# Performance work log

Hardware: AMD Instinct MI355X
Metric: run time of the kernel (lower is better)

## Reference

```python
import jax, jax.numpy as jnp
import numpy as np

N = 100000
E = 1600000
D_IN = 128
D_OUT = 128


def setup_inputs() -> dict:
    key = jax.random.key(0)
    k1, k2, k3, k4 = jax.random.split(key, 4)
    x = jax.random.normal(k1, (N, D_IN), dtype=jnp.float32)
    edge_index = jax.random.randint(k2, (2, E), 0, N, dtype=jnp.int64)
    edge_weight = jax.random.uniform(k3, (E,), dtype=jnp.float32)
    # PyG Linear (glorot) weight stored as [in, out] so that xw = x @ weight
    weight = jax.random.normal(k4, (D_IN, D_OUT), dtype=jnp.float32) * (1.0 / np.sqrt(D_IN))
    bias = jnp.zeros((D_OUT,), dtype=jnp.float32)
    prelu_a = jnp.full((1,), 0.25, dtype=jnp.float32)  # nn.PReLU default
    return {"x": x, "edge_index": edge_index, "edge_weight": edge_weight,
            "weight": weight, "bias": bias, "prelu_a": prelu_a}


def _gcn_forward(x, edge_index, edge_weight, weight, bias, prelu_a):
    n = x.shape[0]
    # Linear transform first (PyG GCNConv applies lin before propagate)
    xw = x @ weight  # [N, D_OUT]

    # gcn_norm: add self-loops with weight 1.0
    loop = jnp.arange(n, dtype=edge_index.dtype)
    row = jnp.concatenate([edge_index[0], loop])  # source
    col = jnp.concatenate([edge_index[1], loop])  # target
    ew = jnp.concatenate([edge_weight, jnp.ones((n,), dtype=edge_weight.dtype)])

    # symmetric normalization: deg computed at targets
    deg = jax.ops.segment_sum(ew, col, num_segments=n)  # [N]
    dinv = jnp.where(deg > 0, jax.lax.rsqrt(deg), 0.0)
    norm = dinv[row] * ew * dinv[col]  # [E+N]

    # gather-scale-scatter aggregation
    msgs = norm[:, None] * xw[row]  # [E+N, D_OUT]
    out = jax.ops.segment_sum(msgs, col, num_segments=n) + bias

    # PReLU (single shared slope)
    return jnp.where(out >= 0, out, prelu_a[0] * out)


def reference(x, edge_index, edge_weight, weight, bias, prelu_a):
    return _gcn_forward(x, edge_index, edge_weight, weight, bias, prelu_a)
```

## Files before the change

### kernel.cpp

```cpp
#include <hip/hip_runtime.h>
#include <hip/hip_bf16.h>

#define D 128
#define NBMAX 512
#define CURPAD 16
#define BCAP 6144

typedef __attribute__((ext_vector_type(8))) short bf16x8;
typedef __attribute__((ext_vector_type(4))) float f32x4;

__device__ inline unsigned short f2bf(float f) {
    unsigned u = __float_as_uint(f);
    u = (u + 0x7FFFu + ((u >> 16) & 1u)) >> 16;
    return (unsigned short)u;
}
__device__ inline float bf2f_lo(unsigned u) { return __uint_as_float(u << 16); }
__device__ inline float bf2f_hi(unsigned u) { return __uint_as_float(u & 0xFFFF0000u); }

__global__ __launch_bounds__(512) void prep(int* __restrict__ bcursor, int NB,
                                            const float* __restrict__ W,
                                            bf16x8* __restrict__ gW,
                                            const float* __restrict__ bias,
                                            float* __restrict__ bias_perm) {
    int tid = threadIdx.x;
    if (blockIdx.x == 0) {
        for (int i = tid; i < NB * CURPAD; i += 512) bcursor[i] = 0;
        if (tid < 128) {
            int l = tid >> 3, j = tid & 7;
            bias_perm[tid] = bias[l + 16 * j];
        }
    } else {
        for (int idx = tid; idx < 2048; idx += 512) {
            int tile = idx >> 6;
            int ln   = idx & 63;
            int kt   = tile >> 3;
            int ct   = tile & 7;
            int k0   = kt * 32 + (ln >> 4) * 8;
            int nn   = ct * 16 + (ln & 15);
            bf16x8 v;
            #pragma unroll
            for (int j = 0; j < 8; ++j) v[j] = (short)f2bf(W[(k0 + j) * D + nn]);
            gW[idx] = v;
        }
    }
}

__global__ __launch_bounds__(1024) void phase1(const int* __restrict__ rowi,
                                               const int* __restrict__ coli,
                                               const float* __restrict__ ew,
                                               int* __restrict__ bcursor,
                                               int2* __restrict__ tmp, int E) {
    __shared__ int hist[4][NBMAX];
    __shared__ int runbase[4][NBMAX];
    int tid = threadIdx.x;
    int par = tid >> 8;
    for (int i = tid; i < 4 * NBMAX; i += 1024) ((int*)hist)[i] = 0;
    __syncthreads();
    int base = blockIdx.x * 8192 + tid * 8;
    int col[8], row[8], rank[8]; float w[8];
    if (base + 8 <= E) {
        int4 c0 = *(const int4*)(coli + base), c1 = *(const int4*)(coli + base + 4);
        int4 r0 = *(const int4*)(rowi + base), r1 = *(const int4*)(rowi + base + 4);
        float4 w0 = *(const float4*)(ew + base), w1 = *(const float4*)(ew + base + 4);
        col[0]=c0.x; col[1]=c0.y; col[2]=c0.z; col[3]=c0.w;
        col[4]=c1.x; col[5]=c1.y; col[6]=c1.z; col[7]=c1.w;
        row[0]=r0.x; row[1]=r0.y; row[2]=r0.z; row[3]=r0.w;
        row[4]=r1.x; row[5]=r1.y; row[6]=r1.z; row[7]=r1.w;
        w[0]=w0.x; w[1]=w0.y; w[2]=w0.z; w[3]=w0.w;
        w[4]=w1.x; w[5]=w1.y; w[6]=w1.z; w[7]=w1.w;
    } else {
        #pragma unroll
        for (int j = 0; j < 8; ++j) {
            int e = base + j;
            if (e < E) { col[j] = coli[e]; row[j] = rowi[e]; w[j] = ew[e]; }
            else       { col[j] = -1; }
        }
    }
    #pragma unroll
    for (int j = 0; j < 8; ++j) {
        if (col[j] >= 0) rank[j] = atomicAdd(&hist[par][col[j] >> 8], 1);
    }
    __syncthreads();
    for (int i = tid; i < NBMAX; i += 1024) {
        int c0 = hist[0][i], c1 = hist[1][i], c2 = hist[2][i], c3 = hist[3][i];
        int tot = c0 + c1 + c2 + c3;
        int b = tot ? atomicAdd(&bcursor[i * CURPAD], tot) : 0;
        runbase[0][i] = b;
        runbase[1][i] = b + c0;
        runbase[2][i] = b + c0 + c1;
        runbase[3][i] = b + c0 + c1 + c2;
    }
    __syncthreads();
    #pragma unroll
    for (int j = 0; j < 8; ++j) {
        if (col[j] >= 0) {
            int b = col[j] >> 8;
            int off = runbase[par][b] + rank[j];
            if (off < BCAP)
                tmp[(size_t)b * BCAP + off] =
                    make_int2(((col[j] & 255) << 24) | row[j], __float_as_int(w[j]));
        }
    }
}

__global__ __launch_bounds__(256) void phase2(int2* __restrict__ tmp,
                                              const int* __restrict__ bcursor,
                                              int* __restrict__ rowptr, int* __restrict__ cnt,
                                              float* __restrict__ dinv, int N) {
    __shared__ int2 ebuf[BCAP];
    __shared__ unsigned int cnt_s[2][256];
    __shared__ unsigned long long deg_s[2][256];
    __shared__ int scan_s[256];
    __shared__ int cur[2][256];
    int tid = threadIdx.x;
    int par = tid >> 7;
    cnt_s[0][tid] = 0; cnt_s[1][tid] = 0;
    deg_s[0][tid] = 0; deg_s[1][tid] = 0;
    __syncthreads();
    int b = blockIdx.x;
    int count = bcursor[b * CURPAD]; if (count > BCAP) count = BCAP;
    int gbase = b * BCAP;
    for (int e = tid * 2; e < count; e += 512) {
        if (e + 1 < count) {
            int4 q = *(const int4*)(tmp + gbase + e);
            int2 v0 = make_int2(q.x, q.y), v1 = make_int2(q.z, q.w);
            ebuf[e] = v0; ebuf[e + 1] = v1;
            unsigned cof0 = ((unsigned)v0.x) >> 24, cof1 = ((unsigned)v1.x) >> 24;
            atomicAdd(&cnt_s[par][cof0], 1u);
            atomicAdd(&cnt_s[par][cof1], 1u);
            atomicAdd(&deg_s[par][cof0],
                (unsigned long long)(__int_as_float(v0.y) * 1048576.0f + 0.5f));
            atomicAdd(&deg_s[par][cof1],
                (unsigned long long)(__int_as_float(v1.y) * 1048576.0f + 0.5f));
        } else {
            int2 v = tmp[gbase + e];
            ebuf[e] = v;
            unsigned cof = ((unsigned)v.x) >> 24;
            atomicAdd(&cnt_s[par][cof], 1u);
            atomicAdd(&deg_s[par][cof],
                (unsigned long long)(__int_as_float(v.y) * 1048576.0f + 0.5f));
        }
    }
    __syncthreads();
    int c0 = (int)cnt_s[0][tid];
    int v0 = c0 + (int)cnt_s[1][tid];
    scan_s[tid] = v0; __syncthreads();
    for (int off = 1; off < 256; off <<= 1) {
        int t = (tid >= off) ? scan_s[tid - off] : 0;
        __syncthreads(); scan_s[tid] += t; __syncthreads();
    }
    int excl = scan_s[tid] - v0;
    int node = b * 256 + tid;
    if (node < N) {
        rowptr[node] = gbase + excl;
        cnt[node] = v0;
        unsigned long long dsum = deg_s[0][tid] + deg_s[1][tid];
        float deg = 1.0f + (float)((double)dsum * (1.0 / 1048576.0));
        dinv[node] = rsqrtf(deg);
    }
    cur[0][tid] = gbase + excl;
    cur[1][tid] = gbase + excl + c0;
    __syncthreads();
    int glimit = gbase + count;
    for (int e = tid * 2; e < count; e += 512) {
        int2 v = ebuf[e];
        unsigned coff = ((unsigned)v.x) >> 24;
        int pos = atomicAdd(&cur[par][coff], 1);
        if (pos < glimit) tmp[pos] = make_int2(v.x & 0xFFFFFF, v.y);
        if (e + 1 < count) {
            int2 v1 = ebuf[e + 1];
            unsigned cof1 = ((unsigned)v1.x) >> 24;
            int pos1 = atomicAdd(&cur[par][cof1], 1);
            if (pos1 < glimit) tmp[pos1] = make_int2(v1.x & 0xFFFFFF, v1.y);
        }
    }
}

__global__ __launch_bounds__(256) void gemm_mfma(const float* __restrict__ x,
                                                 const bf16x8* __restrict__ gW,
                                                 const float* __restrict__ dinv,
                                                 unsigned short* __restrict__ yw, int N) {
    int tid  = threadIdx.x;
    int wid  = tid >> 6;
    int lane = tid & 63;
    int quad = lane >> 4;
    int m16  = lane & 15;
    int row0 = blockIdx.x * 64 + wid * 16;
    int row  = row0 + m16;

    f32x4 acc[8];
    #pragma unroll
    for (int ct = 0; ct < 8; ++ct) acc[ct] = (f32x4){0.f, 0.f, 0.f, 0.f};

    #pragma unroll
    for (int kt = 0; kt < 4; ++kt) {
        bf16x8 a;
        if (row < N) {
            const float* xp = x + (size_t)row * D + kt * 32 + quad * 8;
            float4 u0 = *(const float4*)xp;
            float4 u1 = *(const float4*)(xp + 4);
            a[0] = (short)f2bf(u0.x); a[1] = (short)f2bf(u0.y);
            a[2] = (short)f2bf(u0.z); a[3] = (short)f2bf(u0.w);
            a[4] = (short)f2bf(u1.x); a[5] = (short)f2bf(u1.y);
            a[6] = (short)f2bf(u1.z); a[7] = (short)f2bf(u1.w);
        } else {
            #pragma unroll
            for (int j = 0; j < 8; ++j) a[j] = 0;
        }
        #pragma unroll
        for (int ct = 0; ct < 8; ++ct) {
            acc[ct] = __builtin_amdgcn_mfma_f32_16x16x32_bf16(
                a, gW[(kt * 8 + ct) * 64 + lane], acc[ct], 0, 0, 0);
        }
    }

    int rq = row0 + quad * 4;
    #pragma unroll
    for (int i = 0; i < 4; ++i) {
        int r = rq + i;
        if (r < N) {
            float sc = dinv[r];
            unsigned p0 = (unsigned)f2bf(sc * acc[0][i]) | ((unsigned)f2bf(sc * acc[1][i]) << 16);
            unsigned p1 = (unsigned)f2bf(sc * acc[2][i]) | ((unsigned)f2bf(sc * acc[3][i]) << 16);
            unsigned p2 = (unsigned)f2bf(sc * acc[4][i]) | ((unsigned)f2bf(sc * acc[5][i]) << 16);
            unsigned p3 = (unsigned)f2bf(sc * acc[6][i]) | ((unsigned)f2bf(sc * acc[7][i]) << 16);
            *(uint4*)(yw + (size_t)r * D + m16 * 8) = make_uint4(p0, p1, p2, p3);
        }
    }
}

__global__ __launch_bounds__(256) void aggregate(const unsigned short* __restrict__ yw,
                                                 const float* __restrict__ dinv,
                                                 const int* __restrict__ rowptr,
                                                 const int* __restrict__ cnt,
                                                 const int2* __restrict__ sorted,
                                                 const float* __restrict__ bias_perm,
                                                 const float* __restrict__ prelu_a,
                                                 float* __restrict__ out, int N) {
    int wid  = threadIdx.x >> 6;
    int lane = threadIdx.x & 63;
    int n = blockIdx.x * 4 + wid;
    if (n >= N) return;
    int g = lane >> 4;
    int l = lane & 15;
    float2 a0 = {0.f,0.f}, a1 = {0.f,0.f}, a2 = {0.f,0.f}, a3 = {0.f,0.f};
    int s = rowptr[n];
    int cn = cnt[n];
    for (int base = 0; base < cn; base += 64) {
        int rem = cn - base;
        int m = rem < 64 ? rem : 64;
        int2 er = make_int2(0, 0);
        if (lane < rem) er = sorted[s + base + lane];
        float ewv = __int_as_float(er.y);
        int idx = g;
        int   r0 = __shfl(er.x, idx);
        float w0 = __shfl(ewv, idx);
        if (idx >= m) w0 = 0.f;
        uint4 v0 = *(const uint4*)(yw + (size_t)r0 * D + l * 8);
        for (int j = 4; j < m; j += 4) {
            int idx1 = j + g;
            int   r1 = __shfl(er.x, idx1);
            float w1 = __shfl(ewv, idx1);
            if (idx1 >= m) w1 = 0.f;
            uint4 v1 = *(const uint4*)(yw + (size_t)r1 * D + l * 8);
            a0.x = fmaf(w0, bf2f_lo(v0.x), a0.x); a0.y = fmaf(w0, bf2f_hi(v0.x), a0.y);
            a1.x = fmaf(w0, bf2f_lo(v0.y), a1.x); a1.y = fmaf(w0, bf2f_hi(v0.y), a1.y);
            a2.x = fmaf(w0, bf2f_lo(v0.z), a2.x); a2.y = fmaf(w0, bf2f_hi(v0.z), a2.y);
            a3.x = fmaf(w0, bf2f_lo(v0.w), a3.x); a3.y = fmaf(w0, bf2f_hi(v0.w), a3.y);
            v0 = v1; w0 = w1;
        }
        a0.x = fmaf(w0, bf2f_lo(v0.x), a0.x); a0.y = fmaf(w0, bf2f_hi(v0.x), a0.y);
        a1.x = fmaf(w0, bf2f_lo(v0.y), a1.x); a1.y = fmaf(w0, bf2f_hi(v0.y), a1.y);
        a2.x = fmaf(w0, bf2f_lo(v0.z), a2.x); a2.y = fmaf(w0, bf2f_hi(v0.z), a2.y);
        a3.x = fmaf(w0, bf2f_lo(v0.w), a3.x); a3.y = fmaf(w0, bf2f_hi(v0.w), a3.y);
    }
    a0.x += __shfl_xor(a0.x, 16); a0.y += __shfl_xor(a0.y, 16);
    a1.x += __shfl_xor(a1.x, 16); a1.y += __shfl_xor(a1.y, 16);
    a2.x += __shfl_xor(a2.x, 16); a2.y += __shfl_xor(a2.y, 16);
    a3.x += __shfl_xor(a3.x, 16); a3.y += __shfl_xor(a3.y, 16);
    a0.x += __shfl_xor(a0.x, 32); a0.y += __shfl_xor(a0.y, 32);
    a1.x += __shfl_xor(a1.x, 32); a1.y += __shfl_xor(a1.y, 32);
    a2.x += __shfl_xor(a2.x, 32); a2.y += __shfl_xor(a2.y, 32);
    a3.x += __shfl_xor(a3.x, 32); a3.y += __shfl_xor(a3.y, 32);

    if (lane < 16) {
        uint4 sv = *(const uint4*)(yw + (size_t)n * D + lane * 8);
        a0.x += bf2f_lo(sv.x); a0.y += bf2f_hi(sv.x);
        a1.x += bf2f_lo(sv.y); a1.y += bf2f_hi(sv.y);
        a2.x += bf2f_lo(sv.z); a2.y += bf2f_hi(sv.z);
        a3.x += bf2f_lo(sv.w); a3.y += bf2f_hi(sv.w);
        float di = dinv[n];
        float pa = prelu_a[0];
        float4 b0 = *(const float4*)(bias_perm + lane * 8);
        float4 b1 = *(const float4*)(bias_perm + lane * 8 + 4);
        float av[8] = {a0.x, a0.y, a1.x, a1.y, a2.x, a2.y, a3.x, a3.y};
        float bb[8] = {b0.x, b0.y, b0.z, b0.w, b1.x, b1.y, b1.z, b1.w};
        float* op = out + (size_t)n * D + lane;
        #pragma unroll
        for (int j = 0; j < 8; ++j) {
            float v = fmaf(di, av[j], bb[j]);
            v = (v >= 0.f) ? v : pa * v;
            op[16 * j] = v;
        }
    }
}

extern "C" void kernel_launch(void* const* d_in, const int* in_sizes, int n_in,
                              void* d_out, int out_size, void* d_ws, size_t ws_size,
                              hipStream_t stream) {
    const float* x       = (const float*)d_in[0];
    const int*   ei      = (const int*)d_in[1];
    const float* ew      = (const float*)d_in[2];
    const float* W       = (const float*)d_in[3];
    const float* bias    = (const float*)d_in[4];
    const float* prelu_a = (const float*)d_in[5];
    float* out = (float*)d_out;

    int N = in_sizes[0] / D;
    int E = in_sizes[2];
    const int* rowi = ei;
    const int* coli = ei + E;
    int NB = (N + 255) >> 8;

    char* ws = (char*)d_ws;
    size_t o = 0;
    int2*  tmp = (int2*)(ws + o); o += (size_t)NB * BCAP * 8;
    unsigned short* yw = (unsigned short*)(ws + o); o += (size_t)N * D * 2;
    bf16x8* gW   = (bf16x8*)(ws + o); o += 2048 * 16;
    float* bias_perm = (float*)(ws + o); o += D * 4;
    int* bcursor = (int*)(ws + o); o += (size_t)NB * CURPAD * 4;
    o = (o + 255) & ~(size_t)255;
    int* rowptr  = (int*)(ws + o); o += (size_t)N * 4;
    int* cnt     = (int*)(ws + o); o += (size_t)N * 4;
    float* dinv  = (float*)(ws + o); o += (size_t)N * 4;

    prep<<<2, 512, 0, stream>>>(bcursor, NB, W, gW, bias, bias_perm);
    phase1<<<(E + 8191) / 8192, 1024, 0, stream>>>(rowi, coli, ew, bcursor, tmp, E);
    phase2<<<NB, 256, 0, stream>>>(tmp, bcursor, rowptr, cnt, dinv, N);
    gemm_mfma<<<(N + 63) / 64, 256, 0, stream>>>(x, gW, dinv, yw, N);
    aggregate<<<(N + 3) / 4, 256, 0, stream>>>(yw, dinv, rowptr, cnt, tmp, bias_perm, prelu_a, out, N);
}
```

Before: 228.7 us.

## Drop LDS edge buffer in phase2, sort into separate array, fold prep into phase2

```diff
diff --git a/kernel.cpp b/kernel.cpp
--- a/kernel.cpp
+++ b/kernel.cpp
@@ -4,7 +4,7 @@
 #define D 128
 #define NBMAX 512
 #define CURPAD 16
-#define BCAP 6144
+#define BCAP 4608
 
 typedef __attribute__((ext_vector_type(8))) short bf16x8;
 typedef __attribute__((ext_vector_type(4))) float f32x4;
@@ -17,20 +17,74 @@
 __device__ inline float bf2f_lo(unsigned u) { return __uint_as_float(u << 16); }
 __device__ inline float bf2f_hi(unsigned u) { return __uint_as_float(u & 0xFFFF0000u); }
 
-__global__ __launch_bounds__(512) void prep(int* __restrict__ bcursor, int NB,
-                                            const float* __restrict__ W,
-                                            bf16x8* __restrict__ gW,
-                                            const float* __restrict__ bias,
-                                            float* __restrict__ bias_perm) {
+__global__ __launch_bounds__(1024) void phase1(const int* __restrict__ rowi,
+                                               const int* __restrict__ coli,
+                                               const float* __restrict__ ew,
+                                               int* __restrict__ bcursor,
+                                               int2* __restrict__ tmp, int E) {
+    __shared__ int hist[4][NBMAX];
+    __shared__ int runbase[4][NBMAX];
     int tid = threadIdx.x;
-    if (blockIdx.x == 0) {
-        for (int i = tid; i < NB * CURPAD; i += 512) bcursor[i] = 0;
-        if (tid < 128) {
-            int l = tid >> 3, j = tid & 7;
-            bias_perm[tid] = bias[l + 16 * j];
-        }
+    int par = tid >> 8;
+    for (int i = tid; i < 4 * NBMAX; i += 1024) ((int*)hist)[i] = 0;
+    __syncthreads();
+    int base = blockIdx.x * 4096 + tid * 4;
+    int col[4], row[4], rank[4]; float w[4];
+    if (base + 4 <= E) {
+        int4 c = *(const int4*)(coli + base);
+        int4 r = *(const int4*)(rowi + base);
+        float4 f = *(const float4*)(ew + base);
+        col[0]=c.x; col[1]=c.y; col[2]=c.z; col[3]=c.w;
+        row[0]=r.x; row[1]=r.y; row[2]=r.z; row[3]=r.w;
+        w[0]=f.x; w[1]=f.y; w[2]=f.z; w[3]=f.w;
     } else {
-        for (int idx = tid; idx < 2048; idx += 512) {
+        #pragma unroll
+        for (int j = 0; j < 4; ++j) {
+            int e = base + j;
+            if (e < E) { col[j] = coli[e]; row[j] = rowi[e]; w[j] = ew[e]; }
+            else       { col[j] = -1; }
+        }
+    }
+    #pragma unroll
+    for (int j = 0; j < 4; ++j) {
+        if (col[j] >= 0) rank[j] = atomicAdd(&hist[par][col[j] >> 8], 1);
+    }
+    __syncthreads();
+    for (int i = tid; i < NBMAX; i += 1024) {
+        int c0 = hist[0][i], c1 = hist[1][i], c2 = hist[2][i], c3 = hist[3][i];
+        int tot = c0 + c1 + c2 + c3;
+        int b = tot ? atomicAdd(&bcursor[i * CURPAD], tot) : 0;
+        runbase[0][i] = b;
+        runbase[1][i] = b + c0;
+        runbase[2][i] = b + c0 + c1;
+        runbase[3][i] = b + c0 + c1 + c2;
+    }
+    __syncthreads();
+    #pragma unroll
+    for (int j = 0; j < 4; ++j) {
+        if (col[j] >= 0) {
+            int b = col[j] >> 8;
+            int off = runbase[par][b] + rank[j];
+            if (off < BCAP)
+                tmp[(size_t)b * BCAP + off] =
+                    make_int2(((col[j] & 255) << 24) | row[j], __float_as_int(w[j]));
+        }
+    }
+}
+
+__global__ __launch_bounds__(256) void phase2(const int2* __restrict__ tmp,
+                                              int2* __restrict__ sorted,
+                                              const int* __restrict__ bcursor,
+                                              int* __restrict__ rowptr, int* __restrict__ cnt,
+                                              float* __restrict__ dinv, int N, int NB,
+                                              const float* __restrict__ W,
+                                              bf16x8* __restrict__ gW,
+                                              const float* __restrict__ bias,
+                                              float* __restrict__ bias_perm) {
+    int tid = threadIdx.x;
+    int b = blockIdx.x;
+    if (b == NB) {
+        for (int idx = tid; idx < 2048; idx += 256) {
             int tile = idx >> 6;
             int ln   = idx & 63;
             int kt   = tile >> 3;
@@ -42,103 +96,38 @@
             for (int j = 0; j < 8; ++j) v[j] = (short)f2bf(W[(k0 + j) * D + nn]);
             gW[idx] = v;
         }
-    }
-}
-
-__global__ __launch_bounds__(1024) void phase1(const int* __restrict__ rowi,
-                                               const int* __restrict__ coli,
-                                               const float* __restrict__ ew,
-                                               int* __restrict__ bcursor,
-                                               int2* __restrict__ tmp, int E) {
-    __shared__ int hist[4][NBMAX];
-    __shared__ int runbase[4][NBMAX];
-    int tid = threadIdx.x;
-    int par = tid >> 8;
-    for (int i = tid; i < 4 * NBMAX; i += 1024) ((int*)hist)[i] = 0;
-    __syncthreads();
-    int base = blockIdx.x * 8192 + tid * 8;
-    int col[8], row[8], rank[8]; float w[8];
-    if (base + 8 <= E) {
-        int4 c0 = *(const int4*)(coli + base), c1 = *(const int4*)(coli + base + 4);
-        int4 r0 = *(const int4*)(rowi + base), r1 = *(const int4*)(rowi + base + 4);
-        float4 w0 = *(const float4*)(ew + base), w1 = *(const float4*)(ew + base + 4);
-        col[0]=c0.x; col[1]=c0.y; col[2]=c0.z; col[3]=c0.w;
-        col[4]=c1.x; col[5]=c1.y; col[6]=c1.z; col[7]=c1.w;
-        row[0]=r0.x; row[1]=r0.y; row[2]=r0.z; row[3]=r0.w;
-        row[4]=r1.x; row[5]=r1.y; row[6]=r1.z; row[7]=r1.w;
-        w[0]=w0.x; w[1]=w0.y; w[2]=w0.z; w[3]=w0.w;
-        w[4]=w1.x; w[5]=w1.y; w[6]=w1.z; w[7]=w1.w;
-    } else {
-        #pragma unroll
-        for (int j = 0; j < 8; ++j) {
-            int e = base + j;
-            if (e < E) { col[j] = coli[e]; row[j] = rowi[e]; w[j] = ew[e]; }
-            else       { col[j] = -1; }
-        }
-    }
-    #pragma unroll
-    for (int j = 0; j < 8; ++j) {
-        if (col[j] >= 0) rank[j] = atomicAdd(&hist[par][col[j] >> 8], 1);
-    }
-    __syncthreads();
-    for (int i = tid; i < NBMAX; i += 1024) {
-        int c0 = hist[0][i], c1 = hist[1][i], c2 = hist[2][i], c3 = hist[3][i];
-        int tot = c0 + c1 + c2 + c3;
-        int b = tot ? atomicAdd(&bcursor[i * CURPAD], tot) : 0;
-        runbase[0][i] = b;
-        runbase[1][i] = b + c0;
-        runbase[2][i] = b + c0 + c1;
-        runbase[3][i] = b + c0 + c1 + c2;
-    }
-    __syncthreads();
-    #pragma unroll
-    for (int j = 0; j < 8; ++j) {
-        if (col[j] >= 0) {
-            int b = col[j] >> 8;
-            int off = runbase[par][b] + rank[j];
-            if (off < BCAP)
-                tmp[(size_t)b * BCAP + off] =
-                    make_int2(((col[j] & 255) << 24) | row[j], __float_as_int(w[j]));
-        }
-    }
-}
-
-__global__ __launch_bounds__(256) void phase2(int2* __restrict__ tmp,
-                                              const int* __restrict__ bcursor,
-                                              int* __restrict__ rowptr, int* __restrict__ cnt,
-                                              float* __restrict__ dinv, int N) {
-    __shared__ int2 ebuf[BCAP];
+        if (tid < 128) {
+            int l = tid >> 3, j = tid & 7;
+            bias_perm[tid] = bias[l + 16 * j];
+        }
+        return;
+    }
     __shared__ unsigned int cnt_s[2][256];
     __shared__ unsigned long long deg_s[2][256];
     __shared__ int scan_s[256];
     __shared__ int cur[2][256];
-    int tid = threadIdx.x;
     int par = tid >> 7;
     cnt_s[0][tid] = 0; cnt_s[1][tid] = 0;
     deg_s[0][tid] = 0; deg_s[1][tid] = 0;
     __syncthreads();
-    int b = blockIdx.x;
     int count = bcursor[b * CURPAD]; if (count > BCAP) count = BCAP;
     int gbase = b * BCAP;
-    for (int e = tid * 2; e < count; e += 512) {
-        if (e + 1 < count) {
-            int4 q = *(const int4*)(tmp + gbase + e);
-            int2 v0 = make_int2(q.x, q.y), v1 = make_int2(q.z, q.w);
-            ebuf[e] = v0; ebuf[e + 1] = v1;
-            unsigned cof0 = ((unsigned)v0.x) >> 24, cof1 = ((unsigned)v1.x) >> 24;
-            atomicAdd(&cnt_s[par][cof0], 1u);
-            atomicAdd(&cnt_s[par][cof1], 1u);
-            atomicAdd(&deg_s[par][cof0],
-                (unsigned long long)(__int_as_float(v0.y) * 1048576.0f + 0.5f));
-            atomicAdd(&deg_s[par][cof1],
-                (unsigned long long)(__int_as_float(v1.y) * 1048576.0f + 0.5f));
+    for (int e0 = tid * 4; e0 < count; e0 += 1024) {
+        int m = count - e0; if (m > 4) m = 4;
+        int2 v[4];
+        if (m == 4) {
+            int4 q0 = *(const int4*)(tmp + gbase + e0);
+            int4 q1 = *(const int4*)(tmp + gbase + e0 + 2);
+            v[0] = make_int2(q0.x, q0.y); v[1] = make_int2(q0.z, q0.w);
+            v[2] = make_int2(q1.x, q1.y); v[3] = make_int2(q1.z, q1.w);
         } else {
-            int2 v = tmp[gbase + e];
-            ebuf[e] = v;
-            unsigned cof = ((unsigned)v.x) >> 24;
+            for (int j = 0; j < m; ++j) v[j] = tmp[gbase + e0 + j];
+        }
+        for (int j = 0; j < m; ++j) {
+            unsigned cof = ((unsigned)v[j].x) >> 24;
             atomicAdd(&cnt_s[par][cof], 1u);
             atomicAdd(&deg_s[par][cof],
-                (unsigned long long)(__int_as_float(v.y) * 1048576.0f + 0.5f));
+                (unsigned long long)(__int_as_float(v[j].y) * 1048576.0f + 0.5f));
         }
     }
     __syncthreads();
@@ -162,16 +151,21 @@
     cur[1][tid] = gbase + excl + c0;
     __syncthreads();
     int glimit = gbase + count;
-    for (int e = tid * 2; e < count; e += 512) {
-        int2 v = ebuf[e];
-        unsigned coff = ((unsigned)v.x) >> 24;
-        int pos = atomicAdd(&cur[par][coff], 1);
-        if (pos < glimit) tmp[pos] = make_int2(v.x & 0xFFFFFF, v.y);
-        if (e + 1 < count) {
-            int2 v1 = ebuf[e + 1];
-            unsigned cof1 = ((unsigned)v1.x) >> 24;
-            int pos1 = atomicAdd(&cur[par][cof1], 1);
-            if (pos1 < glimit) tmp[pos1] = make_int2(v1.x & 0xFFFFFF, v1.y);
+    for (int e0 = tid * 4; e0 < count; e0 += 1024) {
+        int m = count - e0; if (m > 4) m = 4;
+        int2 v[4];
+        if (m == 4) {
+            int4 q0 = *(const int4*)(tmp + gbase + e0);
+            int4 q1 = *(const int4*)(tmp + gbase + e0 + 2);
+            v[0] = make_int2(q0.x, q0.y); v[1] = make_int2(q0.z, q0.w);
+            v[2] = make_int2(q1.x, q1.y); v[3] = make_int2(q1.z, q1.w);
+        } else {
+            for (int j = 0; j < m; ++j) v[j] = tmp[gbase + e0 + j];
+        }
+        for (int j = 0; j < m; ++j) {
+            unsigned cof = ((unsigned)v[j].x) >> 24;
+            int pos = atomicAdd(&cur[par][cof], 1);
+            if (pos < glimit) sorted[pos] = make_int2(v[j].x & 0xFFFFFF, v[j].y);
         }
     }
 }
@@ -324,8 +318,14 @@
 
     char* ws = (char*)d_ws;
     size_t o = 0;
-    int2*  tmp = (int2*)(ws + o); o += (size_t)NB * BCAP * 8;
-    unsigned short* yw = (unsigned short*)(ws + o); o += (size_t)N * D * 2;
+    int2* sorted = (int2*)(ws + o); o += (size_t)NB * BCAP * 8;
+    size_t xbase = o;
+    int2* tmp = (int2*)(ws + xbase);
+    unsigned short* yw = (unsigned short*)(ws + xbase);
+    size_t tmp_sz = (size_t)NB * BCAP * 8;
+    size_t yw_sz  = (size_t)N * D * 2;
+    o += (tmp_sz > yw_sz ? tmp_sz : yw_sz);
+    o = (o + 255) & ~(size_t)255;
     bf16x8* gW   = (bf16x8*)(ws + o); o += 2048 * 16;
     float* bias_perm = (float*)(ws + o); o += D * 4;
     int* bcursor = (int*)(ws + o); o += (size_t)NB * CURPAD * 4;
@@ -334,9 +334,10 @@
     int* cnt     = (int*)(ws + o); o += (size_t)N * 4;
     float* dinv  = (float*)(ws + o); o += (size_t)N * 4;
 
-    prep<<<2, 512, 0, stream>>>(bcursor, NB, W, gW, bias, bias_perm);
-    phase1<<<(E + 8191) / 8192, 1024, 0, stream>>>(rowi, coli, ew, bcursor, tmp, E);
-    phase2<<<NB, 256, 0, stream>>>(tmp, bcursor, rowptr, cnt, dinv, N);
+    hipMemsetAsync(bcursor, 0, (size_t)NB * CURPAD * 4, stream);
+    phase1<<<(E + 4095) / 4096, 1024, 0, stream>>>(rowi, coli, ew, bcursor, tmp, E);
+    phase2<<<NB + 1, 256, 0, stream>>>(tmp, sorted, bcursor, rowptr, cnt, dinv, N, NB,
+                                       W, gW, bias, bias_perm);
     gemm_mfma<<<(N + 63) / 64, 256, 0, stream>>>(x, gW, dinv, yw, N);
-    aggregate<<<(N + 3) / 4, 256, 0, stream>>>(yw, dinv, rowptr, cnt, tmp, bias_perm, prelu_a, out, N);
-}
+    aggregate<<<(N + 3) / 4, 256, 0, stream>>>(yw, dinv, rowptr, cnt, sorted, bias_perm, prelu_a, out, N);
+}
```

New measurement: 266.2 us. 16.4% more time.

## Fuse GEMM into bucket-sort phase2 and fold prep into phase1

Applied to the files above, without the earlier changes.

```diff
diff --git a/kernel.cpp b/kernel.cpp
--- a/kernel.cpp
+++ b/kernel.cpp
@@ -17,20 +17,18 @@
 __device__ inline float bf2f_lo(unsigned u) { return __uint_as_float(u << 16); }
 __device__ inline float bf2f_hi(unsigned u) { return __uint_as_float(u & 0xFFFF0000u); }
 
-__global__ __launch_bounds__(512) void prep(int* __restrict__ bcursor, int NB,
-                                            const float* __restrict__ W,
-                                            bf16x8* __restrict__ gW,
-                                            const float* __restrict__ bias,
-                                            float* __restrict__ bias_perm) {
+__global__ __launch_bounds__(1024) void phase1(const int* __restrict__ rowi,
+                                               const int* __restrict__ coli,
+                                               const float* __restrict__ ew,
+                                               int* __restrict__ bcursor,
+                                               int2* __restrict__ tmp, int E, int nbE,
+                                               const float* __restrict__ W,
+                                               bf16x8* __restrict__ gW,
+                                               const float* __restrict__ bias,
+                                               float* __restrict__ bias_perm) {
     int tid = threadIdx.x;
-    if (blockIdx.x == 0) {
-        for (int i = tid; i < NB * CURPAD; i += 512) bcursor[i] = 0;
-        if (tid < 128) {
-            int l = tid >> 3, j = tid & 7;
-            bias_perm[tid] = bias[l + 16 * j];
-        }
-    } else {
-        for (int idx = tid; idx < 2048; idx += 512) {
+    if (blockIdx.x == nbE) {
+        for (int idx = tid; idx < 2048; idx += 1024) {
             int tile = idx >> 6;
             int ln   = idx & 63;
             int kt   = tile >> 3;
@@ -42,17 +40,14 @@
             for (int j = 0; j < 8; ++j) v[j] = (short)f2bf(W[(k0 + j) * D + nn]);
             gW[idx] = v;
         }
-    }
-}
-
-__global__ __launch_bounds__(1024) void phase1(const int* __restrict__ rowi,
-                                               const int* __restrict__ coli,
-                                               const float* __restrict__ ew,
-                                               int* __restrict__ bcursor,
-                                               int2* __restrict__ tmp, int E) {
+        if (tid < 128) {
+            int l = tid >> 3, j = tid & 7;
+            bias_perm[tid] = bias[l + 16 * j];
+        }
+        return;
+    }
     __shared__ int hist[4][NBMAX];
     __shared__ int runbase[4][NBMAX];
-    int tid = threadIdx.x;
     int par = tid >> 8;
     for (int i = tid; i < 4 * NBMAX; i += 1024) ((int*)hist)[i] = 0;
     __syncthreads();
@@ -106,12 +101,16 @@
 __global__ __launch_bounds__(256) void phase2(int2* __restrict__ tmp,
                                               const int* __restrict__ bcursor,
                                               int* __restrict__ rowptr, int* __restrict__ cnt,
-                                              float* __restrict__ dinv, int N) {
+                                              float* __restrict__ dinv, int N,
+                                              const float* __restrict__ x,
+                                              const bf16x8* __restrict__ gW,
+                                              unsigned short* __restrict__ yw) {
     __shared__ int2 ebuf[BCAP];
     __shared__ unsigned int cnt_s[2][256];
     __shared__ unsigned long long deg_s[2][256];
     __shared__ int scan_s[256];
     __shared__ int cur[2][256];
+    __shared__ float dinv_s[256];
     int tid = threadIdx.x;
     int par = tid >> 7;
     cnt_s[0][tid] = 0; cnt_s[1][tid] = 0;
@@ -151,12 +150,16 @@
     }
     int excl = scan_s[tid] - v0;
     int node = b * 256 + tid;
-    if (node < N) {
-        rowptr[node] = gbase + excl;
-        cnt[node] = v0;
+    {
         unsigned long long dsum = deg_s[0][tid] + deg_s[1][tid];
         float deg = 1.0f + (float)((double)dsum * (1.0 / 1048576.0));
-        dinv[node] = rsqrtf(deg);
+        float dv = rsqrtf(deg);
+        dinv_s[tid] = dv;
+        if (node < N) {
+            rowptr[node] = gbase + excl;
+            cnt[node] = v0;
+            dinv[node] = dv;
+        }
     }
     cur[0][tid] = gbase + excl;
     cur[1][tid] = gbase + excl + c0;
@@ -174,57 +177,55 @@
             if (pos1 < glimit) tmp[pos1] = make_int2(v1.x & 0xFFFFFF, v1.y);
         }
     }
-}
-
-__global__ __launch_bounds__(256) void gemm_mfma(const float* __restrict__ x,
-                                                 const bf16x8* __restrict__ gW,
-                                                 const float* __restrict__ dinv,
-                                                 unsigned short* __restrict__ yw, int N) {
-    int tid  = threadIdx.x;
+    __syncthreads();
+
+    bf16x8* smW = (bf16x8*)ebuf;
+    for (int idx = tid; idx < 2048; idx += 256) smW[idx] = gW[idx];
+    __syncthreads();
     int wid  = tid >> 6;
     int lane = tid & 63;
     int quad = lane >> 4;
     int m16  = lane & 15;
-    int row0 = blockIdx.x * 64 + wid * 16;
-    int row  = row0 + m16;
-
-    f32x4 acc[8];
     #pragma unroll
-    for (int ct = 0; ct < 8; ++ct) acc[ct] = (f32x4){0.f, 0.f, 0.f, 0.f};
-
-    #pragma unroll
-    for (int kt = 0; kt < 4; ++kt) {
-        bf16x8 a;
-        if (row < N) {
-            const float* xp = x + (size_t)row * D + kt * 32 + quad * 8;
-            float4 u0 = *(const float4*)xp;
-            float4 u1 = *(const float4*)(xp + 4);
-            a[0] = (short)f2bf(u0.x); a[1] = (short)f2bf(u0.y);
-            a[2] = (short)f2bf(u0.z); a[3] = (short)f2bf(u0.w);
-            a[4] = (short)f2bf(u1.x); a[5] = (short)f2bf(u1.y);
-            a[6] = (short)f2bf(u1.z); a[7] = (short)f2bf(u1.w);
-        } else {
+    for (int rb = 0; rb < 4; ++rb) {
+        int row0 = b * 256 + rb * 64 + wid * 16;
+        int row  = row0 + m16;
+        f32x4 acc[8];
+        #pragma unroll
+        for (int ct = 0; ct < 8; ++ct) acc[ct] = (f32x4){0.f, 0.f, 0.f, 0.f};
+        #pragma unroll
+        for (int kt = 0; kt < 4; ++kt) {
+            bf16x8 a;
+            if (row < N) {
+                const float* xp = x + (size_t)row * D + kt * 32 + quad * 8;
+                float4 u0 = *(const float4*)xp;
+                float4 u1 = *(const float4*)(xp + 4);
+                a[0] = (short)f2bf(u0.x); a[1] = (short)f2bf(u0.y);
+                a[2] = (short)f2bf(u0.z); a[3] = (short)f2bf(u0.w);
+                a[4] = (short)f2bf(u1.x); a[5] = (short)f2bf(u1.y);
+                a[6] = (short)f2bf(u1.z); a[7] = (short)f2bf(u1.w);
+            } else {
+                #pragma unroll
+                for (int j = 0; j < 8; ++j) a[j] = 0;
+            }
             #pragma unroll
-            for (int j = 0; j < 8; ++j) a[j] = 0;
-        }
-        #pragma unroll
-        for (int ct = 0; ct < 8; ++ct) {
-            acc[ct] = __builtin_amdgcn_mfma_f32_16x16x32_bf16(
-                a, gW[(kt * 8 + ct) * 64 + lane], acc[ct], 0, 0, 0);
-        }
-    }
-
-    int rq = row0 + quad * 4;
-    #pragma unroll
-    for (int i = 0; i < 4; ++i) {
-        int r = rq + i;
-        if (r < N) {
-            float sc = dinv[r];
-            unsigned p0 = (unsigned)f2bf(sc * acc[0][i]) | ((unsigned)f2bf(sc * acc[1][i]) << 16);
-            unsigned p1 = (unsigned)f2bf(sc * acc[2][i]) | ((unsigned)f2bf(sc * acc[3][i]) << 16);
-            unsigned p2 = (unsigned)f2bf(sc * acc[4][i]) | ((unsigned)f2bf(sc * acc[5][i]) << 16);
-            unsigned p3 = (unsigned)f2bf(sc * acc[6][i]) | ((unsigned)f2bf(sc * acc[7][i]) << 16);
-            *(uint4*)(yw + (size_t)r * D + m16 * 8) = make_uint4(p0, p1, p2, p3);
+            for (int ct = 0; ct < 8; ++ct) {
+                acc[ct] = __builtin_amdgcn_mfma_f32_16x16x32_bf16(
+                    a, smW[(kt * 8 + ct) * 64 + lane], acc[ct], 0, 0, 0);
+            }
+        }
+        int rq = row0 + quad * 4;
+        #pragma unroll
+        for (int i = 0; i < 4; ++i) {
+            int r = rq + i;
+            if (r < N) {
+                float sc = dinv_s[r - b * 256];
+                unsigned p0 = (unsigned)f2bf(sc * acc[0][i]) | ((unsigned)f2bf(sc * acc[1][i]) << 16);
+                unsigned p1 = (unsigned)f2bf(sc * acc[2][i]) | ((unsigned)f2bf(sc * acc[3][i]) << 16);
+                unsigned p2 = (unsigned)f2bf(sc * acc[4][i]) | ((unsigned)f2bf(sc * acc[5][i]) << 16);
+                unsigned p3 = (unsigned)f2bf(sc * acc[6][i]) | ((unsigned)f2bf(sc * acc[7][i]) << 16);
+                *(uint4*)(yw + (size_t)r * D + m16 * 8) = make_uint4(p0, p1, p2, p3);
+            }
         }
     }
 }
@@ -321,6 +322,7 @@
     const int* rowi = ei;
     const int* coli = ei + E;
     int NB = (N + 255) >> 8;
+    int nbE = (E + 8191) / 8192;
 
     char* ws = (char*)d_ws;
     size_t o = 0;
@@ -334,9 +336,9 @@
     int* cnt     = (int*)(ws + o); o += (size_t)N * 4;
     float* dinv  = (float*)(ws + o); o += (size_t)N * 4;
 
-    prep<<<2, 512, 0, stream>>>(bcursor, NB, W, gW, bias, bias_perm);
-    phase1<<<(E + 8191) / 8192, 1024, 0, stream>>>(rowi, coli, ew, bcursor, tmp, E);
-    phase2<<<NB, 256, 0, stream>>>(tmp, bcursor, rowptr, cnt, dinv, N);
-    gemm_mfma<<<(N + 63) / 64, 256, 0, stream>>>(x, gW, dinv, yw, N);
+    hipMemsetAsync(bcursor, 0, (size_t)NB * CURPAD * 4, stream);
+    phase1<<<nbE + 1, 1024, 0, stream>>>(rowi, coli, ew, bcursor, tmp, E, nbE,
+                                         W, gW, bias, bias_perm);
+    phase2<<<NB, 256, 0, stream>>>(tmp, bcursor, rowptr, cnt, dinv, N, x, gW, yw);
     aggregate<<<(N + 3) / 4, 256, 0, stream>>>(yw, dinv, rowptr, cnt, tmp, bias_perm, prelu_a, out, N);
 }
```

Measured after the change: 219.1 us. 4.2% less time.
